# Performance work log

Measured on AMD Instinct MI355X. Metric: run time of the kernel, lower is better.

Reference implementation:

```python
import jax, jax.numpy as jnp
import numpy as np
import math

HEAD_SIZE = 128
N_EMBED = 2048
B, T = 4, 4096
TOP_K_RATIO = 0.1


def setup_inputs() -> dict:
    key = jax.random.key(0)
    k1, k2, k3, k4 = jax.random.split(key, 4)
    index = jax.random.normal(k1, (B, T, N_EMBED), dtype=jnp.float32)
    s = 1.0 / math.sqrt(N_EMBED)
    Wq = jax.random.normal(k2, (N_EMBED, HEAD_SIZE), dtype=jnp.float32) * s
    Wk = jax.random.normal(k3, (N_EMBED, HEAD_SIZE), dtype=jnp.float32) * s
    Wv = jax.random.normal(k4, (N_EMBED, HEAD_SIZE), dtype=jnp.float32) * s
    return {"index": index, "Wq": Wq, "Wk": Wk, "Wv": Wv}


def reference(index, Wq, Wk, Wv):
    # memory = index (self-attention case)
    Bv, Tv, _ = index.shape
    top_k = int(TOP_K_RATIO * Tv)  # 409

    q = index @ Wq  # [B, T, D]
    k = index @ Wk
    v = index @ Wv

    q_norms = jnp.linalg.norm(q, axis=-1)  # [B, T]
    _, top_idx = jax.lax.top_k(q_norms, top_k)  # [B, K]

    idx = top_idx[..., None]  # [B, K, 1]
    q_topk = jnp.take_along_axis(q, idx, axis=1)  # [B, K, D]
    k_topk = jnp.take_along_axis(k, idx, axis=1)
    v_topk = jnp.take_along_axis(v, idx, axis=1)

    w = jnp.einsum('bid,bjd->bij', q_topk, k_topk) / math.sqrt(HEAD_SIZE)
    # eval mode: no causal mask (only applied in training), dropout = identity
    w = jax.nn.softmax(w, axis=-1)  # stable softmax (internal max subtraction)
    out_topk = w @ v_topk  # [B, K, D]

    batch_idx = jnp.arange(Bv)[:, None]  # [B, 1]
    output = jnp.zeros((Bv, Tv, HEAD_SIZE), dtype=out_topk.dtype)
    output = output.at[batch_idx, top_idx].add(out_topk)  # scatter_add (indices unique)
    return output
```

## Files before the change

kernel.cpp:

```cpp
#include <hip/hip_runtime.h>
#include <hip/hip_bf16.h>

#define NB 4
#define NT 4096
#define NC 2048
#define ND 128
#define NK 409
#define KPAD 416
#define NM (NB * NK)

typedef __attribute__((ext_vector_type(8))) short short8;
typedef __attribute__((ext_vector_type(4))) float f32x4;

union S8U { short8 v; ushort u[8]; };

__device__ __forceinline__ void split2(float x, ushort& h, ushort& l) {
    union { float f; unsigned u; } a; a.f = x;
    unsigned r = a.u + 0x7FFFu + ((a.u >> 16) & 1u);
    h = (ushort)(r >> 16);
    union { unsigned u; float f; } hb; hb.u = ((unsigned)h) << 16;
    float res = x - hb.f;
    union { float f; unsigned u; } b; b.f = res;
    unsigned r2 = b.u + 0x7FFFu + ((b.u >> 16) & 1u);
    l = (ushort)(r2 >> 16);
}

__device__ __forceinline__ uint4 pack8(const ushort* s) {
    uint4 v;
    v.x = (unsigned)s[0] | ((unsigned)s[1] << 16);
    v.y = (unsigned)s[2] | ((unsigned)s[3] << 16);
    v.z = (unsigned)s[4] | ((unsigned)s[5] << 16);
    v.w = (unsigned)s[6] | ((unsigned)s[7] << 16);
    return v;
}

__device__ __forceinline__ int slotOf(int n, int lq) {
    return n * 4 + ((lq + (n >> 1)) & 3);
}

__global__ __launch_bounds__(256) void bconv_tiles(
    const float* __restrict__ W, ushort* __restrict__ Bt)
{
    const int kt = blockIdx.x;
    const int t = threadIdx.x;
    const int n = t & 127;
    const int lq0 = (t >> 7) * 2;
    #pragma unroll
    for (int e = 0; e < 2; ++e) {
        int lq = lq0 + e;
        ushort h[8], l[8];
        #pragma unroll
        for (int j = 0; j < 8; ++j) {
            float x = W[(size_t)(kt * 32 + lq * 8 + j) * ND + n];
            split2(x, h[j], l[j]);
        }
        int slot = slotOf(n, lq);
        *(uint4*)&Bt[((size_t)(kt * 2 + 0) * 512 + slot) * 8] = pack8(h);
        *(uint4*)&Bt[((size_t)(kt * 2 + 1) * 512 + slot) * 8] = pack8(l);
    }
}

#define QSTEP(BHC, BLC, BHN, BLN, KT)                                         \
    {                                                                         \
        short8 ah, al;                                                        \
        {                                                                     \
            S8U H, L;                                                         \
            float xs[8] = {fa0.x, fa0.y, fa0.z, fa0.w,                        \
                           fa1.x, fa1.y, fa1.z, fa1.w};                       \
            _Pragma("unroll")                                                 \
            for (int j = 0; j < 8; ++j) split2(xs[j], H.u[j], L.u[j]);        \
            ah = H.v; al = L.v;                                               \
        }                                                                     \
        const int ktn = ((KT) + 1 < KITER) ? (KT) + 1 : (KT);                 \
        const ushort* gbn = Bt + (size_t)(kt0 + ktn) * 8192;                  \
        _Pragma("unroll")                                                     \
        for (int ni = 0; ni < 8; ++ni) {                                      \
            BHN[ni] = *(const short8*)(gbn + boff[ni]);                       \
            BLN[ni] = *(const short8*)(gbn + 4096 + boff[ni]);                \
        }                                                                     \
        fa0 = *(const float4*)(arow + ktn * 32);                              \
        fa1 = *(const float4*)(arow + ktn * 32 + 4);                          \
        _Pragma("unroll")                                                     \
        for (int ni = 0; ni < 8; ++ni) {                                      \
            acc[ni] = __builtin_amdgcn_mfma_f32_16x16x32_bf16(ah, BHC[ni], acc[ni], 0, 0, 0); \
            acc[ni] = __builtin_amdgcn_mfma_f32_16x16x32_bf16(ah, BLC[ni], acc[ni], 0, 0, 0); \
            acc[ni] = __builtin_amdgcn_mfma_f32_16x16x32_bf16(al, BHC[ni], acc[ni], 0, 0, 0); \
        }                                                                     \
    }

#define QSPLIT 2
__global__ __launch_bounds__(512, 4) void qgemm_v7(
    const float* __restrict__ A, const ushort* __restrict__ Bt,
    float* __restrict__ q1, float* __restrict__ q2)
{
    __shared__ __align__(16) float RED[4][64][32];

    const int tid = threadIdx.x;
    const int w = tid >> 6, lane = tid & 63;
    const int rg = w & 3, kh = w >> 2;
    const int lrow = lane & 15, lq = lane >> 4;
    const int m0 = blockIdx.x * 64;
    const int KITER = 16;
    const int kt0 = (blockIdx.y * 2 + kh) * 16;
    const int kb = blockIdx.y * 1024 + kh * 512;

    const float* arow = A + (size_t)(m0 + rg * 16 + lrow) * NC + kb + lq * 8;

    int boff[8];
    #pragma unroll
    for (int ni = 0; ni < 8; ++ni)
        boff[ni] = slotOf(ni * 16 + lrow, lq) * 8;

    f32x4 acc[8];
    #pragma unroll
    for (int i = 0; i < 8; ++i) acc[i] = (f32x4){0.f, 0.f, 0.f, 0.f};

    short8 bhA[8], blA[8], bhB[8], blB[8];
    {
        const ushort* gb = Bt + (size_t)kt0 * 8192;
        #pragma unroll
        for (int ni = 0; ni < 8; ++ni) {
            bhA[ni] = *(const short8*)(gb + boff[ni]);
            blA[ni] = *(const short8*)(gb + 4096 + boff[ni]);
        }
    }
    float4 fa0 = *(const float4*)(arow + 0);
    float4 fa1 = *(const float4*)(arow + 4);

    for (int kt = 0; kt < KITER; kt += 2) {
        QSTEP(bhA, blA, bhB, blB, kt);
        QSTEP(bhB, blB, bhA, blA, kt + 1);
    }

    if (kh == 1) {
        #pragma unroll
        for (int c = 0; c < 8; ++c) {
            int ch = (c + lane) & 7;
            *(f32x4*)&RED[rg][lane][ch * 4] = acc[ch];
        }
    }
    __syncthreads();
    if (kh == 0) {
        #pragma unroll
        for (int c = 0; c < 8; ++c) {
            int ch = (c + lane) & 7;
            f32x4 o = *(const f32x4*)&RED[rg][lane][ch * 4];
            acc[ch][0] += o[0]; acc[ch][1] += o[1];
            acc[ch][2] += o[2]; acc[ch][3] += o[3];
        }
        float* __restrict__ qd = blockIdx.y ? q2 : q1;
        #pragma unroll
        for (int ni = 0; ni < 8; ++ni) {
            const int col = ni * 16 + lrow;
            #pragma unroll
            for (int r = 0; r < 4; ++r) {
                const int grow = m0 + rg * 16 + lq * 4 + r;
                qd[(size_t)grow * ND + col] = acc[ni][r];
            }
        }
    }
}

#define KVSPLIT 8
__global__ __launch_bounds__(256) void kvgemm_v5(
    const float* __restrict__ X, const ushort* __restrict__ Bkt,
    const ushort* __restrict__ Bvt, const int* __restrict__ topi,
    float* __restrict__ ktop, float* __restrict__ vtop)
{
    const int tid = threadIdx.x;
    const int w = tid >> 6, lane = tid & 63;
    const int lrow = lane & 15, lq = lane >> 4;
    const int m0 = blockIdx.x * 64;
    const int KITER = (NC / KVSPLIT) / 32;
    const int kt0 = blockIdx.y * KITER;
    const int kb = blockIdx.y * (NC / KVSPLIT);
    const ushort* __restrict__ Bt = blockIdx.z ? Bvt : Bkt;

    const int gi = m0 + w * 16 + lrow;
    const int giC = gi < NM ? gi : NM - 1;
    const int b = giC / NK, ii = giC % NK;
    const int src = topi[b * KPAD + ii];
    const float* arow = X + ((size_t)b * NT + src) * NC + kb + lq * 8;

    int boff[8];
    #pragma unroll
    for (int ni = 0; ni < 8; ++ni)
        boff[ni] = slotOf(ni * 16 + lrow, lq) * 8;

    f32x4 acc[8];
    #pragma unroll
    for (int i = 0; i < 8; ++i) acc[i] = (f32x4){0.f, 0.f, 0.f, 0.f};

    short8 bhA[8], blA[8], bhB[8], blB[8];
    {
        const ushort* gb = Bt + (size_t)kt0 * 8192;
        #pragma unroll
        for (int ni = 0; ni < 8; ++ni) {
            bhA[ni] = *(const short8*)(gb + boff[ni]);
            blA[ni] = *(const short8*)(gb + 4096 + boff[ni]);
        }
    }
    float4 fa0 = *(const float4*)(arow + 0);
    float4 fa1 = *(const float4*)(arow + 4);

    for (int kt = 0; kt < KITER; kt += 2) {
        QSTEP(bhA, blA, bhB, blB, kt);
        QSTEP(bhB, blB, bhA, blA, kt + 1);
    }

    float* __restrict__ dst = blockIdx.z ? vtop : ktop;
    #pragma unroll
    for (int ni = 0; ni < 8; ++ni) {
        const int col = ni * 16 + lrow;
        #pragma unroll
        for (int r = 0; r < 4; ++r) {
            const int grow = m0 + w * 16 + lq * 4 + r;
            if (grow < NM)
                atomicAdd(&dst[(size_t)grow * ND + col], acc[ni][r]);
        }
    }
}

__global__ __launch_bounds__(256) void qnorm_kernel(
    float* __restrict__ q1, const float* __restrict__ q2, float* __restrict__ qn)
{
    const int wv = (blockIdx.x * 256 + threadIdx.x) >> 6;
    const int lane = threadIdx.x & 63;
    float* r1 = q1 + (size_t)wv * ND;
    const float* r2 = q2 + (size_t)wv * ND;
    float a = r1[lane] + r2[lane];
    float b = r1[lane + 64] + r2[lane + 64];
    r1[lane] = a;
    r1[lane + 64] = b;
    float s = a * a + b * b;
    #pragma unroll
    for (int off = 32; off > 0; off >>= 1) s += __shfl_xor(s, off);
    if (lane == 0) qn[wv] = sqrtf(s);
}

__global__ __launch_bounds__(256) void topk_kernel(
    const float* __restrict__ qn, int* __restrict__ topi, int* __restrict__ cnt)
{
    __shared__ int rs[4][64];
    const int b = blockIdx.y;
    const int is = threadIdx.x & 63;
    const int i = blockIdx.x * 64 + is;
    const int chunk = threadIdx.x >> 6;
    const float vi = qn[(size_t)b * NT + i];
    const float4* qv = (const float4*)(qn + (size_t)b * NT + chunk * 1024);
    int rank = 0;
    #pragma unroll 4
    for (int j4 = 0; j4 < 256; ++j4) {
        float4 v = qv[j4];
        int j = chunk * 1024 + j4 * 4;
        rank += (v.x > vi || (v.x == vi && (j + 0) < i)) ? 1 : 0;
        rank += (v.y > vi || (v.y == vi && (j + 1) < i)) ? 1 : 0;
        rank += (v.z > vi || (v.z == vi && (j + 2) < i)) ? 1 : 0;
        rank += (v.w > vi || (v.w == vi && (j + 3) < i)) ? 1 : 0;
    }
    rs[chunk][is] = rank;
    __syncthreads();
    if (threadIdx.x < 64) {
        int rk = rs[0][threadIdx.x] + rs[1][threadIdx.x] + rs[2][threadIdx.x] + rs[3][threadIdx.x];
        if (rk < NK) {
            int p = atomicAdd(&cnt[b], 1);
            topi[b * KPAD + p] = blockIdx.x * 64 + threadIdx.x;
        }
    }
}

__global__ __launch_bounds__(256) void attn_kernel(
    const float* __restrict__ q, const float* __restrict__ ktop,
    const float* __restrict__ vtop, const int* __restrict__ topi,
    float* __restrict__ out)
{
    __shared__ float qs[ND];
    __shared__ float ss[KPAD];
    __shared__ float red[256];
    __shared__ float pv[2][ND];
    const int bi = blockIdx.x;
    const int b = bi / NK, i = bi % NK;
    const int t = threadIdx.x;
    const int row = topi[b * KPAD + i];
    if (t < ND) qs[t] = q[((size_t)b * NT + row) * ND + t];
    __syncthreads();

    const float scale = 0.08838834764831844f;
    float mymax = -1e30f;
    #pragma unroll
    for (int rep = 0; rep < 2; ++rep) {
        int j = t + rep * 256;
        if (j < NK) {
            const float4* kr = (const float4*)(ktop + ((size_t)b * NK + j) * ND);
            const float4* q4 = (const float4*)qs;
            float s = 0.f;
            #pragma unroll
            for (int dd = 0; dd < 32; ++dd) {
                float4 a = q4[dd], kv = kr[dd];
                s += a.x * kv.x + a.y * kv.y + a.z * kv.z + a.w * kv.w;
            }
            s *= scale;
            ss[j] = s;
            mymax = fmaxf(mymax, s);
        }
    }
    red[t] = mymax;
    __syncthreads();
    for (int off = 128; off > 0; off >>= 1) {
        if (t < off) red[t] = fmaxf(red[t], red[t + off]);
        __syncthreads();
    }
    const float mx = red[0];
    __syncthreads();

    float mysum = 0.f;
    #pragma unroll
    for (int rep = 0; rep < 2; ++rep) {
        int j = t + rep * 256;
        if (j < NK) {
            float p = __expf(ss[j] - mx);
            ss[j] = p;
            mysum += p;
        }
    }
    red[t] = mysum;
    __syncthreads();
    for (int off = 128; off > 0; off >>= 1) {
        if (t < off) red[t] += red[t + off];
        __syncthreads();
    }
    const float inv = 1.f / red[0];

    const int col = t & (ND - 1), half = t >> 7;
    float o = 0.f;
    #pragma unroll 4
    for (int j = half; j < NK; j += 2)
        o = fmaf(ss[j], vtop[((size_t)b * NK + j) * ND + col], o);
    pv[half][col] = o;
    __syncthreads();
    if (t < ND)
        out[((size_t)b * NT + row) * ND + t] = (pv[0][t] + pv[1][t]) * inv;
}

extern "C" void kernel_launch(void* const* d_in, const int* in_sizes, int n_in,
                              void* d_out, int out_size, void* d_ws, size_t ws_size,
                              hipStream_t stream)
{
    const float* index = (const float*)d_in[0];
    const float* Wq = (const float*)d_in[1];
    const float* Wk = (const float*)d_in[2];
    const float* Wv = (const float*)d_in[3];
    float* out = (float*)d_out;

    char* ws = (char*)d_ws;
    float*  q1   = (float*)(ws);
    float*  qn   = (float*)(ws + 8388608);
    int*    topi = (int*)  (ws + 8454144);
    int*    cnt  = (int*)  (ws + 8462336);
    ushort* Bqt  = (ushort*)(ws + 8462592);
    float*  ktop = (float*)(ws + 8462592);
    float*  vtop = (float*)(ws + 9300224);

    float*  q2  = (float*)d_out;
    ushort* Bkt = (ushort*)d_out;
    ushort* Bvt = (ushort*)((char*)d_out + 1048576);

    hipMemsetAsync(cnt, 0, NB * sizeof(int), stream);

    bconv_tiles<<<dim3(64), dim3(256), 0, stream>>>(Wq, Bqt);
    qgemm_v7<<<dim3(NB * NT / 64, QSPLIT), dim3(512), 0, stream>>>(index, Bqt, q1, q2);
    qnorm_kernel<<<dim3(NB * NT / 4), dim3(256), 0, stream>>>(q1, q2, qn);
    topk_kernel<<<dim3(NT / 64, NB), dim3(256), 0, stream>>>(qn, topi, cnt);
    bconv_tiles<<<dim3(64), dim3(256), 0, stream>>>(Wk, Bkt);
    bconv_tiles<<<dim3(64), dim3(256), 0, stream>>>(Wv, Bvt);
    hipMemsetAsync(ktop, 0, 2 * 837632, stream);
    kvgemm_v5<<<dim3((NM + 63) / 64, KVSPLIT, 2), dim3(256), 0, stream>>>(
        index, Bkt, Bvt, topi, ktop, vtop);
    hipMemsetAsync(d_out, 0, (size_t)out_size * sizeof(float), stream);
    attn_kernel<<<dim3(NM), dim3(256), 0, stream>>>(q1, ktop, vtop, topi, out);
}
```

Measured before the change: 396.1 us.

## Swap qgemm/kvgemm split strategies, reorder A prefetch, tile K in shared memory for attention

The Q GEMM drops its intra-block split-K over two wave groups with an LDS reduction and becomes a plain 256-thread kernel over half of K. The gathered K/V GEMM takes over that intra-block split-K design, with KVSPLIT going from 8 to 4, so each block does more work and issues fewer atomics. The A-row prefetch is moved ahead of the B-fragment loads in the MFMA step. The attention score loop now stages 64-row K tiles in padded shared memory and splits each dot product across four thread slices, replacing per-thread strided row reads, at the cost of more barriers.

```diff
diff --git a/kernel.cpp b/kernel.cpp
--- a/kernel.cpp
+++ b/kernel.cpp
@@ -72,14 +72,14 @@
             ah = H.v; al = L.v;                                               \
         }                                                                     \
         const int ktn = ((KT) + 1 < KITER) ? (KT) + 1 : (KT);                 \
+        fa0 = *(const float4*)(arow + ktn * 32);                              \
+        fa1 = *(const float4*)(arow + ktn * 32 + 4);                          \
         const ushort* gbn = Bt + (size_t)(kt0 + ktn) * 8192;                  \
         _Pragma("unroll")                                                     \
         for (int ni = 0; ni < 8; ++ni) {                                      \
             BHN[ni] = *(const short8*)(gbn + boff[ni]);                       \
             BLN[ni] = *(const short8*)(gbn + 4096 + boff[ni]);                \
         }                                                                     \
-        fa0 = *(const float4*)(arow + ktn * 32);                              \
-        fa1 = *(const float4*)(arow + ktn * 32 + 4);                          \
         _Pragma("unroll")                                                     \
         for (int ni = 0; ni < 8; ++ni) {                                      \
             acc[ni] = __builtin_amdgcn_mfma_f32_16x16x32_bf16(ah, BHC[ni], acc[ni], 0, 0, 0); \
@@ -89,9 +89,63 @@
     }
 
 #define QSPLIT 2
-__global__ __launch_bounds__(512, 4) void qgemm_v7(
+__global__ __launch_bounds__(256) void qgemm_v11(
     const float* __restrict__ A, const ushort* __restrict__ Bt,
     float* __restrict__ q1, float* __restrict__ q2)
+{
+    const int tid = threadIdx.x;
+    const int w = tid >> 6, lane = tid & 63;
+    const int lrow = lane & 15, lq = lane >> 4;
+    const int m0 = blockIdx.x * 64;
+    const int KITER = (NC / QSPLIT) / 32;
+    const int kt0 = blockIdx.y * KITER;
+    const int kb = blockIdx.y * (NC / QSPLIT);
+
+    const float* arow = A + (size_t)(m0 + w * 16 + lrow) * NC + kb + lq * 8;
+
+    int boff[8];
+    #pragma unroll
+    for (int ni = 0; ni < 8; ++ni)
+        boff[ni] = slotOf(ni * 16 + lrow, lq) * 8;
+
+    f32x4 acc[8];
+    #pragma unroll
+    for (int i = 0; i < 8; ++i) acc[i] = (f32x4){0.f, 0.f, 0.f, 0.f};
+
+    float4 fa0 = *(const float4*)(arow + 0);
+    float4 fa1 = *(const float4*)(arow + 4);
+    short8 bhA[8], blA[8], bhB[8], blB[8];
+    {
+        const ushort* gb = Bt + (size_t)kt0 * 8192;
+        #pragma unroll
+        for (int ni = 0; ni < 8; ++ni) {
+            bhA[ni] = *(const short8*)(gb + boff[ni]);
+            blA[ni] = *(const short8*)(gb + 4096 + boff[ni]);
+        }
+    }
+
+    for (int kt = 0; kt < KITER; kt += 2) {
+        QSTEP(bhA, blA, bhB, blB, kt);
+        QSTEP(bhB, blB, bhA, blA, kt + 1);
+    }
+
+    float* __restrict__ qd = blockIdx.y ? q2 : q1;
+    #pragma unroll
+    for (int ni = 0; ni < 8; ++ni) {
+        const int col = ni * 16 + lrow;
+        #pragma unroll
+        for (int r = 0; r < 4; ++r) {
+            const int grow = m0 + w * 16 + lq * 4 + r;
+            qd[(size_t)grow * ND + col] = acc[ni][r];
+        }
+    }
+}
+
+#define KVSPLIT 4
+__global__ __launch_bounds__(512, 2) void kvgemm_v12(
+    const float* __restrict__ X, const ushort* __restrict__ Bkt,
+    const ushort* __restrict__ Bvt, const int* __restrict__ topi,
+    float* __restrict__ ktop, float* __restrict__ vtop)
 {
     __shared__ __align__(16) float RED[4][64][32];
 
@@ -100,11 +154,16 @@
     const int rg = w & 3, kh = w >> 2;
     const int lrow = lane & 15, lq = lane >> 4;
     const int m0 = blockIdx.x * 64;
-    const int KITER = 16;
-    const int kt0 = (blockIdx.y * 2 + kh) * 16;
-    const int kb = blockIdx.y * 1024 + kh * 512;
-
-    const float* arow = A + (size_t)(m0 + rg * 16 + lrow) * NC + kb + lq * 8;
+    const int KITER = 8;
+    const int kt0 = blockIdx.y * 16 + kh * 8;
+    const int kb = blockIdx.y * 512 + kh * 256;
+    const ushort* __restrict__ Bt = blockIdx.z ? Bvt : Bkt;
+
+    const int gi = m0 + rg * 16 + lrow;
+    const int giC = gi < NM ? gi : NM - 1;
+    const int b = giC / NK, ii = giC % NK;
+    const int src = topi[b * KPAD + ii];
+    const float* arow = X + ((size_t)b * NT + src) * NC + kb + lq * 8;
 
     int boff[8];
     #pragma unroll
@@ -115,6 +174,8 @@
     #pragma unroll
     for (int i = 0; i < 8; ++i) acc[i] = (f32x4){0.f, 0.f, 0.f, 0.f};
 
+    float4 fa0 = *(const float4*)(arow + 0);
+    float4 fa1 = *(const float4*)(arow + 4);
     short8 bhA[8], blA[8], bhB[8], blB[8];
     {
         const ushort* gb = Bt + (size_t)kt0 * 8192;
@@ -124,8 +185,6 @@
             blA[ni] = *(const short8*)(gb + 4096 + boff[ni]);
         }
     }
-    float4 fa0 = *(const float4*)(arow + 0);
-    float4 fa1 = *(const float4*)(arow + 4);
 
     for (int kt = 0; kt < KITER; kt += 2) {
         QSTEP(bhA, blA, bhB, blB, kt);
@@ -148,75 +207,16 @@
             acc[ch][0] += o[0]; acc[ch][1] += o[1];
             acc[ch][2] += o[2]; acc[ch][3] += o[3];
         }
-        float* __restrict__ qd = blockIdx.y ? q2 : q1;
+        float* __restrict__ dst = blockIdx.z ? vtop : ktop;
         #pragma unroll
         for (int ni = 0; ni < 8; ++ni) {
             const int col = ni * 16 + lrow;
             #pragma unroll
             for (int r = 0; r < 4; ++r) {
                 const int grow = m0 + rg * 16 + lq * 4 + r;
-                qd[(size_t)grow * ND + col] = acc[ni][r];
+                if (grow < NM)
+                    atomicAdd(&dst[(size_t)grow * ND + col], acc[ni][r]);
             }
-        }
-    }
-}
-
-#define KVSPLIT 8
-__global__ __launch_bounds__(256) void kvgemm_v5(
-    const float* __restrict__ X, const ushort* __restrict__ Bkt,
-    const ushort* __restrict__ Bvt, const int* __restrict__ topi,
-    float* __restrict__ ktop, float* __restrict__ vtop)
-{
-    const int tid = threadIdx.x;
-    const int w = tid >> 6, lane = tid & 63;
-    const int lrow = lane & 15, lq = lane >> 4;
-    const int m0 = blockIdx.x * 64;
-    const int KITER = (NC / KVSPLIT) / 32;
-    const int kt0 = blockIdx.y * KITER;
-    const int kb = blockIdx.y * (NC / KVSPLIT);
-    const ushort* __restrict__ Bt = blockIdx.z ? Bvt : Bkt;
-
-    const int gi = m0 + w * 16 + lrow;
-    const int giC = gi < NM ? gi : NM - 1;
-    const int b = giC / NK, ii = giC % NK;
-    const int src = topi[b * KPAD + ii];
-    const float* arow = X + ((size_t)b * NT + src) * NC + kb + lq * 8;
-
-    int boff[8];
-    #pragma unroll
-    for (int ni = 0; ni < 8; ++ni)
-        boff[ni] = slotOf(ni * 16 + lrow, lq) * 8;
-
-    f32x4 acc[8];
-    #pragma unroll
-    for (int i = 0; i < 8; ++i) acc[i] = (f32x4){0.f, 0.f, 0.f, 0.f};
-
-    short8 bhA[8], blA[8], bhB[8], blB[8];
-    {
-        const ushort* gb = Bt + (size_t)kt0 * 8192;
-        #pragma unroll
-        for (int ni = 0; ni < 8; ++ni) {
-            bhA[ni] = *(const short8*)(gb + boff[ni]);
-            blA[ni] = *(const short8*)(gb + 4096 + boff[ni]);
-        }
-    }
-    float4 fa0 = *(const float4*)(arow + 0);
-    float4 fa1 = *(const float4*)(arow + 4);
-
-    for (int kt = 0; kt < KITER; kt += 2) {
-        QSTEP(bhA, blA, bhB, blB, kt);
-        QSTEP(bhB, blB, bhA, blA, kt + 1);
-    }
-
-    float* __restrict__ dst = blockIdx.z ? vtop : ktop;
-    #pragma unroll
-    for (int ni = 0; ni < 8; ++ni) {
-        const int col = ni * 16 + lrow;
-        #pragma unroll
-        for (int r = 0; r < 4; ++r) {
-            const int grow = m0 + w * 16 + lq * 4 + r;
-            if (grow < NM)
-                atomicAdd(&dst[(size_t)grow * ND + col], acc[ni][r]);
         }
     }
 }
@@ -275,6 +275,8 @@
     float* __restrict__ out)
 {
     __shared__ float qs[ND];
+    __shared__ float ks[64][130];
+    __shared__ float prt[64][5];
     __shared__ float ss[KPAD];
     __shared__ float red[256];
     __shared__ float pv[2][ND];
@@ -283,27 +285,41 @@
     const int t = threadIdx.x;
     const int row = topi[b * KPAD + i];
     if (t < ND) qs[t] = q[((size_t)b * NT + row) * ND + t];
-    __syncthreads();
 
     const float scale = 0.08838834764831844f;
+    const int jloc = t & 63, vsl = t >> 6;
     float mymax = -1e30f;
-    #pragma unroll
-    for (int rep = 0; rep < 2; ++rep) {
-        int j = t + rep * 256;
-        if (j < NK) {
-            const float4* kr = (const float4*)(ktop + ((size_t)b * NK + j) * ND);
-            const float4* q4 = (const float4*)qs;
-            float s = 0.f;
-            #pragma unroll
-            for (int dd = 0; dd < 32; ++dd) {
-                float4 a = q4[dd], kv = kr[dd];
-                s += a.x * kv.x + a.y * kv.y + a.z * kv.z + a.w * kv.w;
+
+    const float2* kbase = (const float2*)(ktop + (size_t)b * NK * ND);
+    for (int tile = 0; tile < 7; ++tile) {
+        __syncthreads();
+        #pragma unroll
+        for (int ii = 0; ii < 16; ++ii) {
+            int f = t + 256 * ii;
+            int r = f >> 6, d2 = f & 63;
+            int grow = tile * 64 + r;
+            float2 val = make_float2(0.f, 0.f);
+            if (grow < NK) val = kbase[(size_t)grow * 64 + d2];
+            *(float2*)&ks[r][2 * d2] = val;
+        }
+        __syncthreads();
+        float p = 0.f;
+        #pragma unroll
+        for (int dd = 0; dd < 32; ++dd)
+            p = fmaf(qs[32 * vsl + dd], ks[jloc][32 * vsl + dd], p);
+        prt[jloc][vsl] = p;
+        __syncthreads();
+        if (t < 64) {
+            int j = tile * 64 + t;
+            if (j < NK) {
+                float s = (prt[t][0] + prt[t][1] + prt[t][2] + prt[t][3]) * scale;
+                ss[j] = s;
+                mymax = fmaxf(mymax, s);
             }
-            s *= scale;
-            ss[j] = s;
-            mymax = fmaxf(mymax, s);
-        }
-    }
+        }
+    }
+    __syncthreads();
+
     red[t] = mymax;
     __syncthreads();
     for (int off = 128; off > 0; off >>= 1) {
@@ -368,13 +384,13 @@
     hipMemsetAsync(cnt, 0, NB * sizeof(int), stream);
 
     bconv_tiles<<<dim3(64), dim3(256), 0, stream>>>(Wq, Bqt);
-    qgemm_v7<<<dim3(NB * NT / 64, QSPLIT), dim3(512), 0, stream>>>(index, Bqt, q1, q2);
+    qgemm_v11<<<dim3(NB * NT / 64, QSPLIT), dim3(256), 0, stream>>>(index, Bqt, q1, q2);
     qnorm_kernel<<<dim3(NB * NT / 4), dim3(256), 0, stream>>>(q1, q2, qn);
     topk_kernel<<<dim3(NT / 64, NB), dim3(256), 0, stream>>>(qn, topi, cnt);
     bconv_tiles<<<dim3(64), dim3(256), 0, stream>>>(Wk, Bkt);
     bconv_tiles<<<dim3(64), dim3(256), 0, stream>>>(Wv, Bvt);
     hipMemsetAsync(ktop, 0, 2 * 837632, stream);
-    kvgemm_v5<<<dim3((NM + 63) / 64, KVSPLIT, 2), dim3(256), 0, stream>>>(
+    kvgemm_v12<<<dim3((NM + 63) / 64, KVSPLIT, 2), dim3(512), 0, stream>>>(
         index, Bkt, Bvt, topi, ktop, vtop);
     hipMemsetAsync(d_out, 0, (size_t)out_size * sizeof(float), stream);
     attn_kernel<<<dim3(NM), dim3(256), 0, stream>>>(q1, ktop, vtop, topi, out);
```

After: 389.8 us. About the same (-1.6%).
